# Optimization experiments

Measured on AMD Instinct MI355X. Metric: run time of the kernel, lower is better.

## Reference

```python
import jax, jax.numpy as jnp
import numpy as np

H = 4096          # hidden_size
M = 4096          # num tokens
BLK = 128         # fp8 quant group/block size
EPS = 1e-6
FP8_MAX = 448.0   # float8_e4m3fn max


def fp8_round(x):
    # round-trip through fp8 e4m3 to emulate FP8 storage
    return x.astype(jnp.float8_e4m3fn).astype(jnp.float32)


def rms_norm(x, w, eps=EPS):
    var = jnp.mean(x * x, axis=-1, keepdims=True)
    return x * jax.lax.rsqrt(var + eps) * w


def block_fp8_linear(x, w, wscale):
    # per-token group-128 activation quant + 128x128 block-scaled fp8 GEMM
    m, k = x.shape
    kb = k // BLK
    nb = w.shape[1] // BLK
    xr = x.reshape(m, kb, BLK)
    amax = jnp.max(jnp.abs(xr), axis=-1)                      # [m, kb]
    s = jnp.maximum(amax, 1e-12) / FP8_MAX                    # group scales
    q = fp8_round(xr / s[..., None])                          # fp8 values
    xdq = (q * s[..., None]).reshape(m, k)                    # dequant acts
    # dequantize weight blockwise: w already fp8-valued floats
    wdq = (w.reshape(kb, BLK, nb, BLK) * wscale[:, None, :, None]).reshape(k, nb * BLK)
    return xdq @ wdq


def setup_inputs() -> dict:
    key = jax.random.key(0)
    ks = jax.random.split(key, 8)
    x = jax.random.normal(ks[0], (M, H), dtype=jnp.float32)
    sb = H // BLK
    d = {"x": x}
    for i in range(3):
        w = fp8_round(jax.random.uniform(ks[1 + i], (H, H), dtype=jnp.float32)).T
        d[f"w{i}"] = w
        d[f"ws{i}"] = jax.random.uniform(ks[4 + i], (sb, sb), dtype=jnp.float32)
    for i in range(4):
        d[f"nw{i}"] = jnp.ones((H,), dtype=jnp.float32)
    return d


def reference(x, w0, ws0, w1, ws1, w2, ws2, nw0, nw1, nw2, nw3):
    x = jax.nn.relu(x)
    resid = x
    y = rms_norm(x, nw0)
    x2 = block_fp8_linear(y, w0, ws0)
    resid = x2 + resid
    y2 = rms_norm(resid, nw1)
    x3 = block_fp8_linear(y2, w1, ws1)
    resid = x3 + resid
    y3 = rms_norm(resid, nw2)
    x4 = block_fp8_linear(y3, w2, ws2)
    resid = x4 + resid
    y4 = rms_norm(resid, nw3)
    return y4
```

## Files before the change

### kernel.cpp

```cpp
#include <hip/hip_runtime.h>
#include <stdint.h>

#define H 4096

typedef float v4f __attribute__((ext_vector_type(4)));
typedef long long i64;
typedef long long v2l __attribute__((ext_vector_type(2)));

__device__ __forceinline__ void gload16(const uint8_t* g, uint8_t* l) {
  __builtin_amdgcn_global_load_lds(
      (const __attribute__((address_space(1))) uint8_t*)g,
      (__attribute__((address_space(3))) uint8_t*)l, 16, 0, 0);
}

__device__ __forceinline__ int permpos(int kg) {
  const int kb = kg >> 7, b = kg & 127;
  const int ks = b >> 5, q = (b >> 3) & 3, j = b & 7;
  return kb * 128 + q * 32 + ks * 8 + j;
}

__global__ __launch_bounds__(256) void conv_w_kernel(
    const float* __restrict__ w0, const float* __restrict__ w1,
    const float* __restrict__ w2, uint8_t* __restrict__ o0,
    uint8_t* __restrict__ o1, uint8_t* __restrict__ o2) {
  const float* w = (blockIdx.z == 0) ? w0 : (blockIdx.z == 1 ? w1 : w2);
  uint8_t* o = (blockIdx.z == 0) ? o0 : (blockIdx.z == 1 ? o1 : o2);
  __shared__ uint8_t t[64][68];
  const int tid = threadIdx.x;
  const int k0 = blockIdx.y * 64, n0 = blockIdx.x * 64;
  const int rr = tid >> 4, cc = (tid & 15) * 4;
#pragma unroll
  for (int j = 0; j < 4; ++j) {
    const int r = rr + j * 16;
    v4f f = *(const v4f*)(w + (size_t)(k0 + r) * H + n0 + cc);
    unsigned p = __builtin_amdgcn_cvt_pk_fp8_f32(f.x, f.y, 0, false);
    p = __builtin_amdgcn_cvt_pk_fp8_f32(f.z, f.w, p, true);
    t[cc + 0][r] = p & 0xff;
    t[cc + 1][r] = (p >> 8) & 0xff;
    t[cc + 2][r] = (p >> 16) & 0xff;
    t[cc + 3][r] = p >> 24;
  }
  __syncthreads();
#pragma unroll
  for (int j = 0; j < 4; ++j) {
    const int n = rr + j * 16;
    unsigned p = (unsigned)t[n][cc] | ((unsigned)t[n][cc + 1] << 8) |
                 ((unsigned)t[n][cc + 2] << 16) |
                 ((unsigned)t[n][cc + 3] << 24);
    *(unsigned*)(o + (size_t)(n0 + n) * H + permpos(k0 + cc)) = p;
  }
}

__global__ __launch_bounds__(256) void quant_kernel(
    const float* in, const float* __restrict__ nw, uint8_t* __restrict__ q,
    float* __restrict__ sxT, const int relu) {
  const int row = blockIdx.x, tid = threadIdx.x;
  const v4f* rp = (const v4f*)(in + (size_t)row * H);
  v4f v[4];
  float ss = 0.f;
#pragma unroll
  for (int j = 0; j < 4; ++j) {
    v4f x = rp[j * 256 + tid];
    if (relu) {
      x.x = fmaxf(x.x, 0.f); x.y = fmaxf(x.y, 0.f);
      x.z = fmaxf(x.z, 0.f); x.w = fmaxf(x.w, 0.f);
    }
    v[j] = x;
    ss += x.x * x.x + x.y * x.y + x.z * x.z + x.w * x.w;
  }
#pragma unroll
  for (int o = 32; o > 0; o >>= 1) ss += __shfl_down(ss, o);
  __shared__ float red[4];
  if ((tid & 63) == 0) red[tid >> 6] = ss;
  __syncthreads();
  ss = red[0] + red[1] + red[2] + red[3];
  const float rinv = 1.f / sqrtf(ss * (1.f / H) + 1e-6f);
#pragma unroll
  for (int j = 0; j < 4; ++j) {
    v4f nv = ((const v4f*)nw)[j * 256 + tid];
    v4f y;
    y.x = v[j].x * rinv * nv.x;
    y.y = v[j].y * rinv * nv.y;
    y.z = v[j].z * rinv * nv.z;
    y.w = v[j].w * rinv * nv.w;
    float am = fmaxf(fmaxf(fabsf(y.x), fabsf(y.y)), fmaxf(fabsf(y.z), fabsf(y.w)));
#pragma unroll
    for (int o = 16; o > 0; o >>= 1) am = fmaxf(am, __shfl_xor(am, o, 32));
    const float s = fmaxf(am, 1e-12f) / 448.f;
    unsigned p = __builtin_amdgcn_cvt_pk_fp8_f32(y.x / s, y.y / s, 0, false);
    p = __builtin_amdgcn_cvt_pk_fp8_f32(y.z / s, y.w / s, p, true);
    const int col = (j * 256 + tid) * 4;
    *(unsigned*)(q + (size_t)row * H + permpos(col)) = p;
    if ((tid & 31) == 0)
      sxT[(size_t)(j * 8 + (tid >> 5)) * 4096 + row] = s;
  }
}

__global__ __launch_bounds__(256) void norm_kernel(float* io,
                                                   const float* __restrict__ nw) {
  const int row = blockIdx.x, tid = threadIdx.x;
  v4f* rp = (v4f*)(io + (size_t)row * H);
  v4f v[4];
  float ss = 0.f;
#pragma unroll
  for (int j = 0; j < 4; ++j) {
    v4f x = rp[j * 256 + tid];
    v[j] = x;
    ss += x.x * x.x + x.y * x.y + x.z * x.z + x.w * x.w;
  }
#pragma unroll
  for (int o = 32; o > 0; o >>= 1) ss += __shfl_down(ss, o);
  __shared__ float red[4];
  if ((tid & 63) == 0) red[tid >> 6] = ss;
  __syncthreads();
  ss = red[0] + red[1] + red[2] + red[3];
  const float rinv = 1.f / sqrtf(ss * (1.f / H) + 1e-6f);
#pragma unroll
  for (int j = 0; j < 4; ++j) {
    v4f nv = ((const v4f*)nw)[j * 256 + tid];
    v4f y;
    y.x = v[j].x * rinv * nv.x;
    y.y = v[j].y * rinv * nv.y;
    y.z = v[j].z * rinv * nv.z;
    y.w = v[j].w * rinv * nv.w;
    rp[j * 256 + tid] = y;
  }
}

__global__ __launch_bounds__(256, 4) void gemm_kernel(
    const uint8_t* __restrict__ qa,
    const float* __restrict__ sxT,
    const uint8_t* __restrict__ wt,
    const float* __restrict__ ws,
    const float* resid, float* outp, const int relu) {
  __shared__ __attribute__((aligned(16))) uint8_t sA[16384];
  __shared__ __attribute__((aligned(16))) uint8_t sB[16384];
  __shared__ __attribute__((aligned(16))) float scb[128];
  __shared__ float ws_s[32];

  const int tid = threadIdx.x;
  const int n0 = blockIdx.x * 128, m0 = blockIdx.y * 128;
  if (tid < 32) ws_s[tid] = ws[tid * 32 + blockIdx.x];

  const int wv = tid >> 6, lane = tid & 63;
  const int quad = lane >> 4, l16 = lane & 15;
  const int wm = wv >> 1, wn = wv & 1;

  const int swc = (tid & 7) ^ ((tid >> 3) & 7);
  const uint8_t* gA = qa + (size_t)(m0 + (tid >> 3)) * H + swc * 16;
  const uint8_t* gB = wt + (size_t)(n0 + (tid >> 3)) * H + swc * 16;
  const uint8_t* gS = (const uint8_t*)sxT + (size_t)m0 * 4 + lane * 16;
  uint8_t* lA = sA + wv * 1024;
  uint8_t* lB = sB + wv * 1024;

  int offp[2];
#pragma unroll
  for (int ksp = 0; ksp < 2; ++ksp)
    offp[ksp] = (((quad * 2 + ksp) ^ (l16 & 7)) << 4);
  const int arow = (wm * 64 + l16) * 128;
  const int brow = (wn * 64 + l16) * 128;
  const int scoff = wm * 64 + quad * 4;

  const v4f zf = {0.f, 0.f, 0.f, 0.f};
  v4f acc[4][4];
#pragma unroll
  for (int i = 0; i < 4; ++i)
#pragma unroll
    for (int j = 0; j < 4; ++j) acc[i][j] = zf;

  for (int kb = 0; kb < 32; ++kb) {
#pragma unroll
    for (int i = 0; i < 4; ++i) {
      gload16(gA + (size_t)i * (32 * H), lA + i * 4096);
      gload16(gB + (size_t)i * (32 * H), lB + i * 4096);
    }
    if (wv == 0 && lane < 32) gload16(gS + (size_t)kb * 16384, (uint8_t*)scb);
    gA += 128;
    gB += 128;
    __syncthreads();

    const float wsk = ws_s[kb];
    v2l bf[4][2];
#pragma unroll
    for (int tc = 0; tc < 4; ++tc)
#pragma unroll
      for (int ksp = 0; ksp < 2; ++ksp)
        bf[tc][ksp] = *(const v2l*)(sB + brow + tc * 2048 + offp[ksp]);

#pragma unroll
    for (int tr = 0; tr < 4; ++tr) {
      const v2l a0 = *(const v2l*)(sA + arow + tr * 2048 + offp[0]);
      const v2l a1 = *(const v2l*)(sA + arow + tr * 2048 + offp[1]);
      const v4f s4 = *(const v4f*)(scb + scoff + tr * 16) * wsk;
#pragma unroll
      for (int tc = 0; tc < 4; ++tc) {
        v4f p = __builtin_amdgcn_mfma_f32_16x16x32_fp8_fp8(a0.x, bf[tc][0].x, zf, 0, 0, 0);
        p = __builtin_amdgcn_mfma_f32_16x16x32_fp8_fp8(a0.y, bf[tc][0].y, p, 0, 0, 0);
        p = __builtin_amdgcn_mfma_f32_16x16x32_fp8_fp8(a1.x, bf[tc][1].x, p, 0, 0, 0);
        p = __builtin_amdgcn_mfma_f32_16x16x32_fp8_fp8(a1.y, bf[tc][1].y, p, 0, 0, 0);
        acc[tr][tc] += p * s4;
      }
    }
    __syncthreads();
  }

  const int mB = m0 + wm * 64 + quad * 4;
  const int nB = n0 + wn * 64 + l16;
#pragma unroll
  for (int tr = 0; tr < 4; ++tr) {
#pragma unroll
    for (int r = 0; r < 4; ++r) {
      const size_t rowOff = (size_t)(mB + tr * 16 + r) * H;
#pragma unroll
      for (int tc = 0; tc < 4; ++tc) {
        const size_t idx = rowOff + nB + tc * 16;
        float rv = resid[idx];
        if (relu) rv = fmaxf(rv, 0.f);
        outp[idx] = acc[tr][tc][r] + rv;
      }
    }
  }
}

extern "C" void kernel_launch(void* const* d_in, const int* in_sizes, int n_in,
                              void* d_out, int out_size, void* d_ws, size_t ws_size,
                              hipStream_t stream) {
  const float* x   = (const float*)d_in[0];
  const float* w0  = (const float*)d_in[1];
  const float* ws0 = (const float*)d_in[2];
  const float* w1  = (const float*)d_in[3];
  const float* ws1 = (const float*)d_in[4];
  const float* w2  = (const float*)d_in[5];
  const float* ws2 = (const float*)d_in[6];
  const float* nw0 = (const float*)d_in[7];
  const float* nw1 = (const float*)d_in[8];
  const float* nw2 = (const float*)d_in[9];
  const float* nw3 = (const float*)d_in[10];
  float* R = (float*)d_out;

  uint8_t* base = (uint8_t*)d_ws;
  uint8_t* wq0 = base;
  uint8_t* wq1 = base + ((size_t)16 << 20);
  uint8_t* wq2 = base + ((size_t)32 << 20);
  uint8_t* qa  = base + ((size_t)48 << 20);
  float* sa    = (float*)(base + ((size_t)64 << 20));

  conv_w_kernel<<<dim3(64, 64, 3), 256, 0, stream>>>(w0, w1, w2, wq0, wq1, wq2);

  quant_kernel<<<4096, 256, 0, stream>>>(x, nw0, qa, sa, 1);
  gemm_kernel<<<dim3(32, 32), 256, 0, stream>>>(qa, sa, wq0, ws0, x, R, 1);

  quant_kernel<<<4096, 256, 0, stream>>>(R, nw1, qa, sa, 0);
  gemm_kernel<<<dim3(32, 32), 256, 0, stream>>>(qa, sa, wq1, ws1, R, R, 0);

  quant_kernel<<<4096, 256, 0, stream>>>(R, nw2, qa, sa, 0);
  gemm_kernel<<<dim3(32, 32), 256, 0, stream>>>(qa, sa, wq2, ws2, R, R, 0);

  norm_kernel<<<4096, 256, 0, stream>>>(R, nw3);
}
```

Measured before the change: 685.4 us.

## Vectorize fp8 weight transpose and activation quant stores with contiguous per-thread layout

The weight conversion kernel now handles 128-row K tiles. Each thread packs 8 fp8 values along K with byte permutes, so the LDS transpose and the global writes become 8- and 16-byte vector accesses instead of byte-wise ones. The quant kernel gives each thread 16 contiguous elements, so the group amax needs only a 3-step shuffle within 8 lanes. Each thread then writes its permuted fp8 output as two 8-byte stores instead of scattered 4-byte ones. This cuts memory transactions and shuffle work in the preprocessing kernels, at the cost of more complex index mapping that must still match the GEMM's permuted layout.

```diff
diff --git a/kernel.cpp b/kernel.cpp
--- a/kernel.cpp
+++ b/kernel.cpp
@@ -25,29 +25,41 @@
     uint8_t* __restrict__ o1, uint8_t* __restrict__ o2) {
   const float* w = (blockIdx.z == 0) ? w0 : (blockIdx.z == 1 ? w1 : w2);
   uint8_t* o = (blockIdx.z == 0) ? o0 : (blockIdx.z == 1 ? o1 : o2);
-  __shared__ uint8_t t[64][68];
+  __shared__ __attribute__((aligned(16))) uint8_t buf[64 * 136];
   const int tid = threadIdx.x;
-  const int k0 = blockIdx.y * 64, n0 = blockIdx.x * 64;
-  const int rr = tid >> 4, cc = (tid & 15) * 4;
-#pragma unroll
-  for (int j = 0; j < 4; ++j) {
-    const int r = rr + j * 16;
-    v4f f = *(const v4f*)(w + (size_t)(k0 + r) * H + n0 + cc);
+  const int k0 = blockIdx.y * 128, n0 = blockIdx.x * 64;
+  const int n4 = tid & 15, krun = tid >> 4;
+
+  unsigned dw[8];
+#pragma unroll
+  for (int i = 0; i < 8; ++i) {
+    v4f f = *(const v4f*)(w + (size_t)(k0 + krun * 8 + i) * H + n0 + n4 * 4);
     unsigned p = __builtin_amdgcn_cvt_pk_fp8_f32(f.x, f.y, 0, false);
-    p = __builtin_amdgcn_cvt_pk_fp8_f32(f.z, f.w, p, true);
-    t[cc + 0][r] = p & 0xff;
-    t[cc + 1][r] = (p >> 8) & 0xff;
-    t[cc + 2][r] = (p >> 16) & 0xff;
-    t[cc + 3][r] = p >> 24;
+    dw[i] = __builtin_amdgcn_cvt_pk_fp8_f32(f.z, f.w, p, true);
+  }
+#pragma unroll
+  for (int b = 0; b < 4; ++b) {
+    const unsigned sel1 = 0x0c0c0000u | ((4u + b) << 8) | (unsigned)b;
+    unsigned p01 = __builtin_amdgcn_perm(dw[1], dw[0], sel1);
+    unsigned p23 = __builtin_amdgcn_perm(dw[3], dw[2], sel1);
+    unsigned lo = __builtin_amdgcn_perm(p23, p01, 0x05040100u);
+    unsigned p45 = __builtin_amdgcn_perm(dw[5], dw[4], sel1);
+    unsigned p67 = __builtin_amdgcn_perm(dw[7], dw[6], sel1);
+    unsigned hi = __builtin_amdgcn_perm(p67, p45, 0x05040100u);
+    uint2 kk; kk.x = lo; kk.y = hi;
+    *(uint2*)(buf + (n4 * 4 + b) * 136 + krun * 8) = kk;
   }
   __syncthreads();
-#pragma unroll
-  for (int j = 0; j < 4; ++j) {
-    const int n = rr + j * 16;
-    unsigned p = (unsigned)t[n][cc] | ((unsigned)t[n][cc + 1] << 8) |
-                 ((unsigned)t[n][cc + 2] << 16) |
-                 ((unsigned)t[n][cc + 3] << 24);
-    *(unsigned*)(o + (size_t)(n0 + n) * H + permpos(k0 + cc)) = p;
+
+#pragma unroll
+  for (int it = 0; it < 2; ++it) {
+    const int id = it * 256 + tid;
+    const int n = id >> 3, c = id & 7;
+    const int r0 = 8 * (c & 1) + (c >> 1);
+    uint2 a = *(const uint2*)(buf + n * 136 + r0 * 8);
+    uint2 b = *(const uint2*)(buf + n * 136 + (r0 + 4) * 8);
+    uint4 outv; outv.x = a.x; outv.y = a.y; outv.z = b.x; outv.w = b.y;
+    *(uint4*)(o + (size_t)(n0 + n) * H + k0 + c * 16) = outv;
   }
 }
 
@@ -55,12 +67,12 @@
     const float* in, const float* __restrict__ nw, uint8_t* __restrict__ q,
     float* __restrict__ sxT, const int relu) {
   const int row = blockIdx.x, tid = threadIdx.x;
-  const v4f* rp = (const v4f*)(in + (size_t)row * H);
+  const v4f* rp = (const v4f*)(in + (size_t)row * H) + tid * 4;
   v4f v[4];
   float ss = 0.f;
 #pragma unroll
   for (int j = 0; j < 4; ++j) {
-    v4f x = rp[j * 256 + tid];
+    v4f x = rp[j];
     if (relu) {
       x.x = fmaxf(x.x, 0.f); x.y = fmaxf(x.y, 0.f);
       x.z = fmaxf(x.z, 0.f); x.w = fmaxf(x.w, 0.f);
@@ -75,25 +87,38 @@
   __syncthreads();
   ss = red[0] + red[1] + red[2] + red[3];
   const float rinv = 1.f / sqrtf(ss * (1.f / H) + 1e-6f);
-#pragma unroll
-  for (int j = 0; j < 4; ++j) {
-    v4f nv = ((const v4f*)nw)[j * 256 + tid];
-    v4f y;
-    y.x = v[j].x * rinv * nv.x;
-    y.y = v[j].y * rinv * nv.y;
-    y.z = v[j].z * rinv * nv.z;
-    y.w = v[j].w * rinv * nv.w;
-    float am = fmaxf(fmaxf(fabsf(y.x), fabsf(y.y)), fmaxf(fabsf(y.z), fabsf(y.w)));
-#pragma unroll
-    for (int o = 16; o > 0; o >>= 1) am = fmaxf(am, __shfl_xor(am, o, 32));
-    const float s = fmaxf(am, 1e-12f) / 448.f;
-    unsigned p = __builtin_amdgcn_cvt_pk_fp8_f32(y.x / s, y.y / s, 0, false);
-    p = __builtin_amdgcn_cvt_pk_fp8_f32(y.z / s, y.w / s, p, true);
-    const int col = (j * 256 + tid) * 4;
-    *(unsigned*)(q + (size_t)row * H + permpos(col)) = p;
-    if ((tid & 31) == 0)
-      sxT[(size_t)(j * 8 + (tid >> 5)) * 4096 + row] = s;
-  }
+
+  const v4f* np = ((const v4f*)nw) + tid * 4;
+  v4f y[4];
+  float am = 0.f;
+#pragma unroll
+  for (int j = 0; j < 4; ++j) {
+    v4f nv = np[j];
+    y[j].x = v[j].x * rinv * nv.x;
+    y[j].y = v[j].y * rinv * nv.y;
+    y[j].z = v[j].z * rinv * nv.z;
+    y[j].w = v[j].w * rinv * nv.w;
+    am = fmaxf(am, fmaxf(fmaxf(fabsf(y[j].x), fabsf(y[j].y)),
+                         fmaxf(fabsf(y[j].z), fabsf(y[j].w))));
+  }
+#pragma unroll
+  for (int o = 4; o > 0; o >>= 1) am = fmaxf(am, __shfl_xor(am, o, 8));
+  const float s = fmaxf(am, 1e-12f) / 448.f;
+  unsigned d[4];
+#pragma unroll
+  for (int j = 0; j < 4; ++j) {
+    unsigned p = __builtin_amdgcn_cvt_pk_fp8_f32(y[j].x / s, y[j].y / s, 0, false);
+    d[j] = __builtin_amdgcn_cvt_pk_fp8_f32(y[j].z / s, y[j].w / s, p, true);
+  }
+  uint8_t* base = q + (size_t)row * H + (tid >> 3) * 128;
+  const int u = tid & 7;
+  const int pos0 = (u >> 1) * 8 + (u & 1) * 64;
+  uint2 st;
+  st.x = d[0]; st.y = d[1];
+  *(uint2*)(base + pos0) = st;
+  st.x = d[2]; st.y = d[3];
+  *(uint2*)(base + pos0 + 32) = st;
+  if (u == 0) sxT[(size_t)(tid >> 3) * 4096 + row] = s;
 }
 
 __global__ __launch_bounds__(256) void norm_kernel(float* io,
@@ -245,7 +270,7 @@
   uint8_t* qa  = base + ((size_t)48 << 20);
   float* sa    = (float*)(base + ((size_t)64 << 20));
 
-  conv_w_kernel<<<dim3(64, 64, 3), 256, 0, stream>>>(w0, w1, w2, wq0, wq1, wq2);
+  conv_w_kernel<<<dim3(64, 32, 3), 256, 0, stream>>>(w0, w1, w2, wq0, wq1, wq2);
 
   quant_kernel<<<4096, 256, 0, stream>>>(x, nw0, qa, sa, 1);
   gemm_kernel<<<dim3(32, 32), 256, 0, stream>>>(qa, sa, wq0, ws0, x, R, 1);
```

Measured after the change: 696.3 us. About the same (+1.6%).
